# Kernel tuning notes

Measured on AMD Instinct MI355X. Metric: run time of the kernel, lower is better.

The kernel has to match this reference:

```python
import jax, jax.numpy as jnp
import numpy as np

DIM = 1024
HEADS = 16
HEAD_DIM = DIM // HEADS
EPS = 1e-5


def layer_norm(x, w, b):
    # normalize over last dim (head_dim)
    mu = jnp.mean(x, axis=-1, keepdims=True)
    var = jnp.mean(jnp.square(x - mu), axis=-1, keepdims=True)
    return (x - mu) * jax.lax.rsqrt(var + EPS) * w + b


def setup_inputs() -> dict:
    key = jax.random.key(0)
    ks = jax.random.split(key, 8)
    B, N = 2, 2048
    x = jax.random.normal(ks[0], (B, N, DIM), dtype=jnp.float32)
    mask = jax.random.randint(ks[1], (B, 1, N, N), 0, 2) == 1  # True = masked out
    qkv_w = jax.random.normal(ks[2], (3 * DIM, DIM), dtype=jnp.float32) * (DIM ** -0.5)
    q_norm_w = jnp.ones((HEAD_DIM,), dtype=jnp.float32)
    q_norm_b = jnp.zeros((HEAD_DIM,), dtype=jnp.float32)
    k_norm_w = jnp.ones((HEAD_DIM,), dtype=jnp.float32)
    k_norm_b = jnp.zeros((HEAD_DIM,), dtype=jnp.float32)
    proj_w = jax.random.normal(ks[3], (DIM, DIM), dtype=jnp.float32) * (DIM ** -0.5)
    proj_b = jnp.zeros((DIM,), dtype=jnp.float32)
    return {"x": x, "mask": mask, "qkv_w": qkv_w,
            "q_norm_w": q_norm_w, "q_norm_b": q_norm_b,
            "k_norm_w": k_norm_w, "k_norm_b": k_norm_b,
            "proj_w": proj_w, "proj_b": proj_b}


def reference(x, mask, qkv_w, q_norm_w, q_norm_b, k_norm_w, k_norm_b, proj_w, proj_b):
    B, N, C = x.shape
    H, D = HEADS, HEAD_DIM
    scale = D ** -0.5
    # qkv projection (no bias), split into q,k,v of shape (B,H,N,D)
    qkv = (x @ qkv_w.T).reshape(B, N, 3, H, D).transpose(2, 0, 3, 1, 4)
    q, k, v = qkv[0], qkv[1], qkv[2]
    q = layer_norm(q, q_norm_w, q_norm_b)
    k = layer_norm(k, k_norm_w, k_norm_b)
    q = q * scale
    attn = jnp.einsum("bhnd,bhmd->bhnm", q, k)  # (B,H,N,N)
    attn = jnp.where(mask, -jnp.inf, attn)
    attn = jax.nn.softmax(attn, axis=-1)
    out = jnp.einsum("bhnm,bhmd->bhnd", attn, v)
    out = out.transpose(0, 2, 1, 3).reshape(B, N, C)
    return out @ proj_w.T + proj_b
```

## Files before the change

kernel.cpp:

```cpp
#include <hip/hip_runtime.h>
#include <hip/hip_bf16.h>
#include <math.h>

#define B_    2
#define N_    2048
#define DIM_  1024
#define H_    16
#define HD_   64
#define EPS_  1e-5f
#define SCALE_ 0.125f

typedef __attribute__((ext_vector_type(8))) __bf16 bf16x8;
typedef __attribute__((ext_vector_type(8))) unsigned short ushort8;
typedef __attribute__((ext_vector_type(4))) float f32x4;

__device__ __forceinline__ unsigned short f2bf(float x) {
    unsigned u = __builtin_bit_cast(unsigned, x);
    u += 0x7fff + ((u >> 16) & 1);
    return (unsigned short)(u >> 16);
}
__device__ __forceinline__ float bf2f(unsigned short x) {
    unsigned u = ((unsigned)x) << 16;
    return __builtin_bit_cast(float, u);
}

__device__ __forceinline__ void gl_lds16(const void* g, void* l) {
    __builtin_amdgcn_global_load_lds(
        (const __attribute__((address_space(1))) void*)g,
        (__attribute__((address_space(3))) void*)l, 16, 0, 0);
}

__global__ __launch_bounds__(256) void cast_all_bf16(
    const float* __restrict__ x, const float* __restrict__ qkvw,
    const float* __restrict__ pw, unsigned short* __restrict__ out) {
    int i = (blockIdx.x * 256 + threadIdx.x) * 8;
    const float* src;
    if (i < 4194304) src = x + i;
    else if (i < 7340032) src = qkvw + (i - 4194304);
    else src = pw + (i - 7340032);
    float4 v0 = *(const float4*)src;
    float4 v1 = *(const float4*)(src + 4);
    ushort8 r;
    r[0] = f2bf(v0.x); r[1] = f2bf(v0.y); r[2] = f2bf(v0.z); r[3] = f2bf(v0.w);
    r[4] = f2bf(v1.x); r[5] = f2bf(v1.y); r[6] = f2bf(v1.z); r[7] = f2bf(v1.w);
    *(ushort8*)(out + i) = r;
}

__global__ __launch_bounds__(256) void pack_mask(
    const int* __restrict__ mask, unsigned long long* __restrict__ bm) {
    int w = blockIdx.x * 4 + (threadIdx.x >> 6);
    int lane = threadIdx.x & 63;
    int mv = mask[(size_t)w * 64 + lane];
    unsigned long long bits = __ballot(mv != 0);
    if (lane == 0) bm[w] = bits;
}

template <int WITH_BIAS, int OUT_BF16>
__global__ __launch_bounds__(256) void gemm_bt_mfma(
    const unsigned short* __restrict__ A, const unsigned short* __restrict__ Bw,
    const float* __restrict__ bias, void* __restrict__ Cout, int M, int Ncols,
    int K) {
    __shared__ unsigned short As[128 * 32];
    __shared__ unsigned short Bs[128 * 32];
    const int tid = threadIdx.x;
    const int wave = tid >> 6, lane = tid & 63;
    const int quad = lane >> 4, lcol = lane & 15;
    const int wr = wave >> 1, wc = wave & 1;
    const int row0 = blockIdx.y * 128, col0 = blockIdx.x * 128;

    f32x4 acc[4][4];
#pragma unroll
    for (int i = 0; i < 4; ++i)
#pragma unroll
        for (int j = 0; j < 4; ++j) acc[i][j] = (f32x4){0.f, 0.f, 0.f, 0.f};

    for (int k0 = 0; k0 < K; k0 += 32) {
        __syncthreads();
#pragma unroll
        for (int c = 0; c < 2; ++c) {
            int base = wave * 2048 + c * 1024;
            int myofs = base + lane * 16;
            int r = myofs >> 6;
            int kb = myofs & 63;
            gl_lds16((const char*)A + ((size_t)(row0 + r) * K + k0) * 2 + kb,
                     (char*)As + base);
            gl_lds16((const char*)Bw + ((size_t)(col0 + r) * K + k0) * 2 + kb,
                     (char*)Bs + base);
        }
        __syncthreads();

        bf16x8 af[4], bfr[4];
#pragma unroll
        for (int i = 0; i < 4; ++i) {
            af[i] = *(const bf16x8*)&As[(wr * 64 + i * 16 + lcol) * 32 + quad * 8];
            bfr[i] = *(const bf16x8*)&Bs[(wc * 64 + i * 16 + lcol) * 32 + quad * 8];
        }
#pragma unroll
        for (int i = 0; i < 4; ++i)
#pragma unroll
            for (int j = 0; j < 4; ++j)
                acc[i][j] = __builtin_amdgcn_mfma_f32_16x16x32_bf16(
                    af[i], bfr[j], acc[i][j], 0, 0, 0);
    }

#pragma unroll
    for (int i = 0; i < 4; ++i) {
#pragma unroll
        for (int j = 0; j < 4; ++j) {
            int col = col0 + wc * 64 + j * 16 + lcol;
            float bv = WITH_BIAS ? bias[col] : 0.f;
#pragma unroll
            for (int reg = 0; reg < 4; ++reg) {
                int row = row0 + wr * 64 + i * 16 + quad * 4 + reg;
                float v = acc[i][j][reg] + bv;
                if (OUT_BF16)
                    ((unsigned short*)Cout)[(size_t)row * Ncols + col] = f2bf(v);
                else
                    ((float*)Cout)[(size_t)row * Ncols + col] = v;
            }
        }
    }
}

__global__ __launch_bounds__(256) void qkv_norm_split(
    const unsigned short* __restrict__ qkv, const float* __restrict__ qw,
    const float* __restrict__ qb, const float* __restrict__ kw,
    const float* __restrict__ kb, unsigned short* __restrict__ qo,
    unsigned short* __restrict__ ko) {
    int wid = blockIdx.x * 4 + (threadIdx.x >> 6);
    int lane = threadIdx.x & 63;
    int h = wid & 15;
    int t = (wid >> 4) & 1;
    int bn = wid >> 5;
    int n = bn & (N_ - 1);
    int b = bn >> 11;
    float val = bf2f(qkv[((size_t)bn * 3 + t) * DIM_ + h * 64 + lane]);
    size_t oidx = ((size_t)(b * H_ + h) * N_ + n) * 64 + lane;
    float s = val;
#pragma unroll
    for (int off = 32; off > 0; off >>= 1) s += __shfl_xor(s, off);
    float mu = s * (1.f / 64.f);
    float d = val - mu;
    float s2 = d * d;
#pragma unroll
    for (int off = 32; off > 0; off >>= 1) s2 += __shfl_xor(s2, off);
    float r = rsqrtf(s2 * (1.f / 64.f) + EPS_);
    if (t == 0) {
        qo[oidx] = f2bf((d * r * qw[lane] + qb[lane]) * SCALE_);
    } else {
        ko[oidx] = f2bf(d * r * kw[lane] + kb[lane]);
    }
}

__global__ __launch_bounds__(256) void transpose_v(
    const unsigned short* __restrict__ qkv, unsigned short* __restrict__ vt) {
    __shared__ unsigned short Ts[64 * 65];
    const int tid = threadIdx.x;
    const int bh = blockIdx.y, n0 = blockIdx.x * 64;
    const int b = bh >> 4, h = bh & 15;
    {
        int r = tid >> 2, s = tid & 3;
        const unsigned short* src =
            qkv + ((size_t)(b * N_ + n0 + r) * 3 + 2) * DIM_ + h * 64 + s * 16;
#pragma unroll
        for (int i = 0; i < 16; ++i) Ts[r * 65 + s * 16 + i] = src[i];
    }
    __syncthreads();
    {
        int d = tid >> 2, ks = tid & 3;
        __align__(16) unsigned short tmp[16];
#pragma unroll
        for (int i = 0; i < 16; ++i) tmp[i] = Ts[(ks * 16 + i) * 65 + d];
        unsigned short* dst = vt + (size_t)(bh * 64 + d) * N_ + n0 + ks * 16;
        *(int4*)dst = *(const int4*)&tmp[0];
        *(int4*)(dst + 8) = *(const int4*)&tmp[8];
    }
}

__global__ __launch_bounds__(256) void flash_attn_mfma3(
    const unsigned short* __restrict__ q, const unsigned short* __restrict__ k,
    const unsigned short* __restrict__ vt,
    const unsigned long long* __restrict__ bm, unsigned short* __restrict__ ao) {
    __shared__ unsigned short Qs[128 * 64];
    __shared__ unsigned short Ks[64 * 64];
    __shared__ unsigned short Vts[64 * 64];
    __shared__ unsigned short Ps[4][32 * 72];

    const int tid = threadIdx.x;
    const int wave = tid >> 6, lane = tid & 63;
    const int quad = lane >> 4, lcol = lane & 15;
    const int bh = blockIdx.y, b = bh >> 4, h = bh & 15;
    const int q0 = blockIdx.x * 128;

    {
        const char* qg = (const char*)(q + (size_t)(bh * N_ + q0) * 64);
#pragma unroll
        for (int c = 0; c < 4; ++c) {
            int base = wave * 4096 + c * 1024;
            gl_lds16(qg + base + lane * 16, (char*)Qs + base);
        }
    }
    __syncthreads();

    bf16x8 bq[2][2];
#pragma unroll
    for (int ct = 0; ct < 2; ++ct)
#pragma unroll
        for (int d0 = 0; d0 < 2; ++d0)
            bq[ct][d0] = *(const bf16x8*)&Qs[(wave * 32 + ct * 16 + lcol) * 64 +
                                             d0 * 32 + quad * 8];

    f32x4 oacc[2][4];
    float m_c[2], l_c[2];
#pragma unroll
    for (int ct = 0; ct < 2; ++ct) {
#pragma unroll
        for (int dt = 0; dt < 4; ++dt) oacc[ct][dt] = (f32x4){0.f, 0.f, 0.f, 0.f};
        m_c[ct] = -3.0e38f;
        l_c[ct] = 0.f;
    }

    const unsigned long long* bmq[2];
#pragma unroll
    for (int ct = 0; ct < 2; ++ct)
        bmq[ct] = bm + ((size_t)b * N_ + q0 + wave * 32 + ct * 16 + lcol) * 32;

    const char* kgbase = (const char*)k + (size_t)bh * N_ * 128;
    const char* vtbase = (const char*)vt + (size_t)bh * 64 * N_ * 2;

    for (int k0 = 0; k0 < N_; k0 += 64) {
        __syncthreads();
#pragma unroll
        for (int ci = 0; ci < 2; ++ci) {
            int c = wave * 2 + ci;
            int swz = (c & 3) * 2;
            int key = lane ^ swz;
            gl_lds16(kgbase + (size_t)(k0 + key) * 128 + c * 16,
                     (char*)Ks + c * 1024);
            int d = lane ^ swz;
            gl_lds16(vtbase + ((size_t)d * N_ + k0 + c * 8) * 2,
                     (char*)Vts + c * 1024);
        }
        unsigned long long mw[2];
        const int widx = k0 >> 6;
        mw[0] = bmq[0][widx];
        mw[1] = bmq[1][widx];
        __syncthreads();

        f32x4 sacc[2][4];
#pragma unroll
        for (int ct = 0; ct < 2; ++ct)
#pragma unroll
            for (int kt = 0; kt < 4; ++kt) sacc[ct][kt] = (f32x4){0.f, 0.f, 0.f, 0.f};
#pragma unroll
        for (int kt = 0; kt < 4; ++kt) {
#pragma unroll
            for (int d0 = 0; d0 < 2; ++d0) {
                int p = d0 * 4 + quad;
                bf16x8 ak = *(const bf16x8*)((const char*)Ks + p * 1024 +
                                             (((kt * 16 + lcol) ^ (quad * 2)) << 4));
#pragma unroll
                for (int ct = 0; ct < 2; ++ct)
                    sacc[ct][kt] = __builtin_amdgcn_mfma_f32_16x16x32_bf16(
                        ak, bq[ct][d0], sacc[ct][kt], 0, 0, 0);
            }
        }

#pragma unroll
        for (int ct = 0; ct < 2; ++ct) {
            unsigned long long mq = mw[ct] >> (quad * 4);
            float mloc = -3.0e38f;
#pragma unroll
            for (int kt = 0; kt < 4; ++kt) {
                unsigned nib = (unsigned)(mq >> (kt * 16)) & 0xFu;
#pragma unroll
                for (int reg = 0; reg < 4; ++reg) {
                    float s = ((nib >> reg) & 1u) ? -1e30f : sacc[ct][kt][reg];
                    sacc[ct][kt][reg] = s;
                    mloc = fmaxf(mloc, s);
                }
            }
            mloc = fmaxf(mloc, __shfl_xor(mloc, 16));
            mloc = fmaxf(mloc, __shfl_xor(mloc, 32));
            float mold = m_c[ct];
            float mnew = fmaxf(mold, mloc);
            float alpha = __expf(mold - mnew);
            m_c[ct] = mnew;
            float rs = 0.f;
#pragma unroll
            for (int kt = 0; kt < 4; ++kt) {
                unsigned short us[4];
#pragma unroll
                for (int reg = 0; reg < 4; ++reg) {
                    float p = __expf(sacc[ct][kt][reg] - mnew);
                    rs += p;
                    us[reg] = f2bf(p);
                }
                uint2 pk;
                pk.x = us[0] | ((unsigned)us[1] << 16);
                pk.y = us[2] | ((unsigned)us[3] << 16);
                *(uint2*)&Ps[wave][(ct * 16 + lcol) * 72 + kt * 16 + quad * 4] = pk;
            }
            rs += __shfl_xor(rs, 16);
            rs += __shfl_xor(rs, 32);
            l_c[ct] = l_c[ct] * alpha + rs;
#pragma unroll
            for (int dt = 0; dt < 4; ++dt)
#pragma unroll
                for (int reg = 0; reg < 4; ++reg) oacc[ct][dt][reg] *= alpha;
        }

#pragma unroll
        for (int k2 = 0; k2 < 2; ++k2) {
            bf16x8 pf[2];
#pragma unroll
            for (int ct = 0; ct < 2; ++ct)
                pf[ct] = *(const bf16x8*)&Ps[wave][(ct * 16 + lcol) * 72 +
                                                   k2 * 32 + quad * 8];
#pragma unroll
            for (int dt = 0; dt < 4; ++dt) {
                int p = k2 * 4 + quad;
                bf16x8 vf = *(const bf16x8*)((const char*)Vts + p * 1024 +
                                             (((dt * 16 + lcol) ^ (quad * 2)) << 4));
#pragma unroll
                for (int ct = 0; ct < 2; ++ct)
                    oacc[ct][dt] = __builtin_amdgcn_mfma_f32_16x16x32_bf16(
                        vf, pf[ct], oacc[ct][dt], 0, 0, 0);
            }
        }
    }

#pragma unroll
    for (int ct = 0; ct < 2; ++ct) {
        float inv = 1.f / l_c[ct];
        int row = q0 + wave * 32 + ct * 16 + lcol;
        unsigned short* dst =
            ao + ((size_t)(b * N_ + row)) * DIM_ + h * 64 + quad * 4;
#pragma unroll
        for (int dt = 0; dt < 4; ++dt) {
            unsigned short us[4];
#pragma unroll
            for (int reg = 0; reg < 4; ++reg)
                us[reg] = f2bf(oacc[ct][dt][reg] * inv);
            uint2 pk;
            pk.x = us[0] | ((unsigned)us[1] << 16);
            pk.y = us[2] | ((unsigned)us[3] << 16);
            *(uint2*)(dst + dt * 16) = pk;
        }
    }
}

extern "C" void kernel_launch(void* const* d_in, const int* in_sizes, int n_in,
                              void* d_out, int out_size, void* d_ws,
                              size_t ws_size, hipStream_t stream) {
    const float* x     = (const float*)d_in[0];
    const int*   mask  = (const int*)d_in[1];
    const float* qkv_w = (const float*)d_in[2];
    const float* qnw   = (const float*)d_in[3];
    const float* qnb   = (const float*)d_in[4];
    const float* knw   = (const float*)d_in[5];
    const float* knb   = (const float*)d_in[6];
    const float* pw    = (const float*)d_in[7];
    const float* pb    = (const float*)d_in[8];
    float* out = (float*)d_out;

    char* ws = (char*)d_ws;
    unsigned short* qkv_bf = (unsigned short*)(ws + 0);
    unsigned short* qbuf   = (unsigned short*)(ws + 25165824);
    unsigned short* kbuf   = (unsigned short*)(ws + 33554432);
    unsigned short* vt     = (unsigned short*)(ws + 41943040);
    unsigned short* x_bf   = (unsigned short*)(ws + 50331648);
    unsigned short* qw_bf  = (unsigned short*)(ws + 58720256);
    unsigned short* pw_bf  = (unsigned short*)(ws + 65011712);
    unsigned short* ao_bnc = x_bf;
    unsigned long long* bmask = (unsigned long long*)(ws + 0);

    cast_all_bf16<<<8388608 / 2048, 256, 0, stream>>>(x, qkv_w, pw, x_bf);

    gemm_bt_mfma<0, 1><<<dim3(3072 / 128, 4096 / 128), 256, 0, stream>>>(
        x_bf, qw_bf, nullptr, qkv_bf, B_ * N_, 3 * DIM_, DIM_);

    qkv_norm_split<<<dim3((B_ * N_ * 2 * H_) / 4), 256, 0, stream>>>(
        qkv_bf, qnw, qnb, knw, knb, qbuf, kbuf);

    transpose_v<<<dim3(N_ / 64, B_ * H_), 256, 0, stream>>>(qkv_bf, vt);

    pack_mask<<<(B_ * N_ * (N_ / 64)) / 4, 256, 0, stream>>>(mask, bmask);

    flash_attn_mfma3<<<dim3(N_ / 128, B_ * H_), 256, 0, stream>>>(
        qbuf, kbuf, vt, bmask, ao_bnc);

    gemm_bt_mfma<1, 0><<<dim3(DIM_ / 128, 4096 / 128), 256, 0, stream>>>(
        ao_bnc, pw_bf, pb, out, B_ * N_, DIM_, DIM_);
}
```

Before: 304.7 us.

## Fuse QK layernorm into QKV GEMM epilogue and halve attention query tile

The QKV GEMM epilogue now computes the per-head layernorm for Q and K directly from accumulators and writes head-major Q/K buffers plus a separate V buffer. This removes the separate norm kernel and the round trip through the bf16 qkv buffer. The attention kernel drops from 128 to 64 query rows per block, which doubles the grid and cuts registers, at the cost of reloading K/V tiles twice as often. Softmax now uses exp2 with log2e folded into the Q scale, and bf16 packing uses a perm-based round (round-half-up rather than round-to-even).

```diff
diff --git a/kernel.cpp b/kernel.cpp
--- a/kernel.cpp
+++ b/kernel.cpp
@@ -9,6 +9,7 @@
 #define HD_   64
 #define EPS_  1e-5f
 #define SCALE_ 0.125f
+#define LOG2E_ 1.4426950408889634f
 
 typedef __attribute__((ext_vector_type(8))) __bf16 bf16x8;
 typedef __attribute__((ext_vector_type(8))) unsigned short ushort8;
@@ -19,9 +20,10 @@
     u += 0x7fff + ((u >> 16) & 1);
     return (unsigned short)(u >> 16);
 }
-__device__ __forceinline__ float bf2f(unsigned short x) {
-    unsigned u = ((unsigned)x) << 16;
-    return __builtin_bit_cast(float, u);
+__device__ __forceinline__ unsigned pk2bf(float a, float b) {
+    unsigned ua = __builtin_bit_cast(unsigned, a) + 0x8000u;
+    unsigned ub = __builtin_bit_cast(unsigned, b) + 0x8000u;
+    return __builtin_amdgcn_perm(ub, ua, 0x07060302);
 }
 
 __device__ __forceinline__ void gl_lds16(const void* g, void* l) {
@@ -55,6 +57,120 @@
     if (lane == 0) bm[w] = bits;
 }
 
+__global__ __launch_bounds__(256) void gemm_qkv_ln(
+    const unsigned short* __restrict__ A, const unsigned short* __restrict__ Bw,
+    const float* __restrict__ qnw, const float* __restrict__ qnb,
+    const float* __restrict__ knw, const float* __restrict__ knb,
+    unsigned short* __restrict__ qbuf, unsigned short* __restrict__ kbuf,
+    unsigned short* __restrict__ vbuf) {
+    const int K = DIM_;
+    __shared__ unsigned short As[128 * 32];
+    __shared__ unsigned short Bs[128 * 32];
+    const int tid = threadIdx.x;
+    const int wave = tid >> 6, lane = tid & 63;
+    const int quad = lane >> 4, lcol = lane & 15;
+    const int wr = wave >> 1, wc = wave & 1;
+    const int row0 = blockIdx.y * 128, col0 = blockIdx.x * 128;
+
+    f32x4 acc[4][4];
+#pragma unroll
+    for (int i = 0; i < 4; ++i)
+#pragma unroll
+        for (int j = 0; j < 4; ++j) acc[i][j] = (f32x4){0.f, 0.f, 0.f, 0.f};
+
+    for (int k0 = 0; k0 < K; k0 += 32) {
+        __syncthreads();
+#pragma unroll
+        for (int c = 0; c < 2; ++c) {
+            int base = wave * 2048 + c * 1024;
+            int myofs = base + lane * 16;
+            int r = myofs >> 6;
+            int kb = myofs & 63;
+            gl_lds16((const char*)A + ((size_t)(row0 + r) * K + k0) * 2 + kb,
+                     (char*)As + base);
+            gl_lds16((const char*)Bw + ((size_t)(col0 + r) * K + k0) * 2 + kb,
+                     (char*)Bs + base);
+        }
+        __syncthreads();
+
+        bf16x8 af[4], bfr[4];
+#pragma unroll
+        for (int i = 0; i < 4; ++i) {
+            af[i] = *(const bf16x8*)&As[(wr * 64 + i * 16 + lcol) * 32 + quad * 8];
+            bfr[i] = *(const bf16x8*)&Bs[(wc * 64 + i * 16 + lcol) * 32 + quad * 8];
+        }
+#pragma unroll
+        for (int i = 0; i < 4; ++i)
+#pragma unroll
+            for (int j = 0; j < 4; ++j)
+                acc[i][j] = __builtin_amdgcn_mfma_f32_16x16x32_bf16(
+                    af[i], bfr[j], acc[i][j], 0, 0, 0);
+    }
+
+    const int colbase = col0 + wc * 64;
+    const int t = colbase >> 10;
+    const int h = (colbase & 1023) >> 6;
+
+    if (t < 2) {
+        const float* wv = (t == 0) ? qnw : knw;
+        const float* bv = (t == 0) ? qnb : knb;
+        float wreg[4], breg[4];
+#pragma unroll
+        for (int j = 0; j < 4; ++j) {
+            wreg[j] = wv[j * 16 + lcol];
+            breg[j] = bv[j * 16 + lcol];
+        }
+        const float sc = (t == 0) ? (SCALE_ * LOG2E_) : 1.f;
+        unsigned short* obase = (t == 0) ? qbuf : kbuf;
+#pragma unroll
+        for (int i = 0; i < 4; ++i) {
+#pragma unroll
+            for (int reg = 0; reg < 4; ++reg) {
+                int row = row0 + wr * 64 + i * 16 + quad * 4 + reg;
+                int bb = row >> 11, n = row & (N_ - 1);
+                float v[4];
+#pragma unroll
+                for (int j = 0; j < 4; ++j) v[j] = acc[i][j][reg];
+                float s = v[0] + v[1] + v[2] + v[3];
+                s += __shfl_xor(s, 1);
+                s += __shfl_xor(s, 2);
+                s += __shfl_xor(s, 4);
+                s += __shfl_xor(s, 8);
+                float mu = s * (1.f / 64.f);
+                float d[4], s2 = 0.f;
+#pragma unroll
+                for (int j = 0; j < 4; ++j) {
+                    d[j] = v[j] - mu;
+                    s2 += d[j] * d[j];
+                }
+                s2 += __shfl_xor(s2, 1);
+                s2 += __shfl_xor(s2, 2);
+                s2 += __shfl_xor(s2, 4);
+                s2 += __shfl_xor(s2, 8);
+                float r = rsqrtf(s2 * (1.f / 64.f) + EPS_);
+                unsigned short* dst =
+                    obase + ((size_t)(bb * H_ + h) * N_ + n) * 64 + lcol;
+#pragma unroll
+                for (int j = 0; j < 4; ++j)
+                    dst[j * 16] = f2bf((d[j] * r * wreg[j] + breg[j]) * sc);
+            }
+        }
+    } else {
+        const int dcol = colbase & 1023;
+#pragma unroll
+        for (int i = 0; i < 4; ++i) {
+#pragma unroll
+            for (int reg = 0; reg < 4; ++reg) {
+                int row = row0 + wr * 64 + i * 16 + quad * 4 + reg;
+                unsigned short* dst = vbuf + (size_t)row * DIM_ + dcol + lcol;
+#pragma unroll
+                for (int j = 0; j < 4; ++j)
+                    dst[j * 16] = f2bf(acc[i][j][reg]);
+            }
+        }
+    }
+}
+
 template <int WITH_BIAS, int OUT_BF16>
 __global__ __launch_bounds__(256) void gemm_bt_mfma(
     const unsigned short* __restrict__ A, const unsigned short* __restrict__ Bw,
@@ -122,38 +238,8 @@
     }
 }
 
-__global__ __launch_bounds__(256) void qkv_norm_split(
-    const unsigned short* __restrict__ qkv, const float* __restrict__ qw,
-    const float* __restrict__ qb, const float* __restrict__ kw,
-    const float* __restrict__ kb, unsigned short* __restrict__ qo,
-    unsigned short* __restrict__ ko) {
-    int wid = blockIdx.x * 4 + (threadIdx.x >> 6);
-    int lane = threadIdx.x & 63;
-    int h = wid & 15;
-    int t = (wid >> 4) & 1;
-    int bn = wid >> 5;
-    int n = bn & (N_ - 1);
-    int b = bn >> 11;
-    float val = bf2f(qkv[((size_t)bn * 3 + t) * DIM_ + h * 64 + lane]);
-    size_t oidx = ((size_t)(b * H_ + h) * N_ + n) * 64 + lane;
-    float s = val;
-#pragma unroll
-    for (int off = 32; off > 0; off >>= 1) s += __shfl_xor(s, off);
-    float mu = s * (1.f / 64.f);
-    float d = val - mu;
-    float s2 = d * d;
-#pragma unroll
-    for (int off = 32; off > 0; off >>= 1) s2 += __shfl_xor(s2, off);
-    float r = rsqrtf(s2 * (1.f / 64.f) + EPS_);
-    if (t == 0) {
-        qo[oidx] = f2bf((d * r * qw[lane] + qb[lane]) * SCALE_);
-    } else {
-        ko[oidx] = f2bf(d * r * kw[lane] + kb[lane]);
-    }
-}
-
 __global__ __launch_bounds__(256) void transpose_v(
-    const unsigned short* __restrict__ qkv, unsigned short* __restrict__ vt) {
+    const unsigned short* __restrict__ vbuf, unsigned short* __restrict__ vt) {
     __shared__ unsigned short Ts[64 * 65];
     const int tid = threadIdx.x;
     const int bh = blockIdx.y, n0 = blockIdx.x * 64;
@@ -161,7 +247,7 @@
     {
         int r = tid >> 2, s = tid & 3;
         const unsigned short* src =
-            qkv + ((size_t)(b * N_ + n0 + r) * 3 + 2) * DIM_ + h * 64 + s * 16;
+            vbuf + (size_t)(b * N_ + n0 + r) * DIM_ + h * 64 + s * 16;
 #pragma unroll
         for (int i = 0; i < 16; ++i) Ts[r * 65 + s * 16 + i] = src[i];
     }
@@ -177,54 +263,43 @@
     }
 }
 
-__global__ __launch_bounds__(256) void flash_attn_mfma3(
+__global__ __launch_bounds__(256) void flash_attn_mfma4(
     const unsigned short* __restrict__ q, const unsigned short* __restrict__ k,
     const unsigned short* __restrict__ vt,
     const unsigned long long* __restrict__ bm, unsigned short* __restrict__ ao) {
-    __shared__ unsigned short Qs[128 * 64];
+    __shared__ unsigned short Qs[64 * 64];
     __shared__ unsigned short Ks[64 * 64];
     __shared__ unsigned short Vts[64 * 64];
-    __shared__ unsigned short Ps[4][32 * 72];
+    __shared__ unsigned short Ps[4][16 * 72];
 
     const int tid = threadIdx.x;
     const int wave = tid >> 6, lane = tid & 63;
     const int quad = lane >> 4, lcol = lane & 15;
     const int bh = blockIdx.y, b = bh >> 4, h = bh & 15;
-    const int q0 = blockIdx.x * 128;
+    const int q0 = blockIdx.x * 64;
 
     {
         const char* qg = (const char*)(q + (size_t)(bh * N_ + q0) * 64);
 #pragma unroll
-        for (int c = 0; c < 4; ++c) {
-            int base = wave * 4096 + c * 1024;
+        for (int c = 0; c < 2; ++c) {
+            int base = wave * 2048 + c * 1024;
             gl_lds16(qg + base + lane * 16, (char*)Qs + base);
         }
     }
     __syncthreads();
 
-    bf16x8 bq[2][2];
-#pragma unroll
-    for (int ct = 0; ct < 2; ++ct)
-#pragma unroll
-        for (int d0 = 0; d0 < 2; ++d0)
-            bq[ct][d0] = *(const bf16x8*)&Qs[(wave * 32 + ct * 16 + lcol) * 64 +
-                                             d0 * 32 + quad * 8];
-
-    f32x4 oacc[2][4];
-    float m_c[2], l_c[2];
-#pragma unroll
-    for (int ct = 0; ct < 2; ++ct) {
-#pragma unroll
-        for (int dt = 0; dt < 4; ++dt) oacc[ct][dt] = (f32x4){0.f, 0.f, 0.f, 0.f};
-        m_c[ct] = -3.0e38f;
-        l_c[ct] = 0.f;
-    }
-
-    const unsigned long long* bmq[2];
-#pragma unroll
-    for (int ct = 0; ct < 2; ++ct)
-        bmq[ct] = bm + ((size_t)b * N_ + q0 + wave * 32 + ct * 16 + lcol) * 32;
-
+    bf16x8 bq[2];
+#pragma unroll
+    for (int d0 = 0; d0 < 2; ++d0)
+        bq[d0] = *(const bf16x8*)&Qs[(wave * 16 + lcol) * 64 + d0 * 32 + quad * 8];
+
+    f32x4 oacc[4];
+#pragma unroll
+    for (int dt = 0; dt < 4; ++dt) oacc[dt] = (f32x4){0.f, 0.f, 0.f, 0.f};
+    float m_c = -3.0e38f, l_c = 0.f;
+
+    const unsigned long long* bmq =
+        bm + ((size_t)b * N_ + q0 + wave * 16 + lcol) * 32;
     const char* kgbase = (const char*)k + (size_t)bh * N_ * 128;
     const char* vtbase = (const char*)vt + (size_t)bh * 64 * N_ * 2;
 
@@ -241,17 +316,12 @@
             gl_lds16(vtbase + ((size_t)d * N_ + k0 + c * 8) * 2,
                      (char*)Vts + c * 1024);
         }
-        unsigned long long mw[2];
-        const int widx = k0 >> 6;
-        mw[0] = bmq[0][widx];
-        mw[1] = bmq[1][widx];
-        __syncthreads();
-
-        f32x4 sacc[2][4];
-#pragma unroll
-        for (int ct = 0; ct < 2; ++ct)
-#pragma unroll
-            for (int kt = 0; kt < 4; ++kt) sacc[ct][kt] = (f32x4){0.f, 0.f, 0.f, 0.f};
+        unsigned long long mw = bmq[k0 >> 6];
+        __syncthreads();
+
+        f32x4 sacc[4];
+#pragma unroll
+        for (int kt = 0; kt < 4; ++kt) sacc[kt] = (f32x4){0.f, 0.f, 0.f, 0.f};
 #pragma unroll
         for (int kt = 0; kt < 4; ++kt) {
 #pragma unroll
@@ -259,94 +329,73 @@
                 int p = d0 * 4 + quad;
                 bf16x8 ak = *(const bf16x8*)((const char*)Ks + p * 1024 +
                                              (((kt * 16 + lcol) ^ (quad * 2)) << 4));
-#pragma unroll
-                for (int ct = 0; ct < 2; ++ct)
-                    sacc[ct][kt] = __builtin_amdgcn_mfma_f32_16x16x32_bf16(
-                        ak, bq[ct][d0], sacc[ct][kt], 0, 0, 0);
-            }
-        }
-
-#pragma unroll
-        for (int ct = 0; ct < 2; ++ct) {
-            unsigned long long mq = mw[ct] >> (quad * 4);
-            float mloc = -3.0e38f;
-#pragma unroll
-            for (int kt = 0; kt < 4; ++kt) {
-                unsigned nib = (unsigned)(mq >> (kt * 16)) & 0xFu;
-#pragma unroll
-                for (int reg = 0; reg < 4; ++reg) {
-                    float s = ((nib >> reg) & 1u) ? -1e30f : sacc[ct][kt][reg];
-                    sacc[ct][kt][reg] = s;
-                    mloc = fmaxf(mloc, s);
-                }
-            }
-            mloc = fmaxf(mloc, __shfl_xor(mloc, 16));
-            mloc = fmaxf(mloc, __shfl_xor(mloc, 32));
-            float mold = m_c[ct];
-            float mnew = fmaxf(mold, mloc);
-            float alpha = __expf(mold - mnew);
-            m_c[ct] = mnew;
-            float rs = 0.f;
-#pragma unroll
-            for (int kt = 0; kt < 4; ++kt) {
-                unsigned short us[4];
-#pragma unroll
-                for (int reg = 0; reg < 4; ++reg) {
-                    float p = __expf(sacc[ct][kt][reg] - mnew);
-                    rs += p;
-                    us[reg] = f2bf(p);
-                }
-                uint2 pk;
-                pk.x = us[0] | ((unsigned)us[1] << 16);
-                pk.y = us[2] | ((unsigned)us[3] << 16);
-                *(uint2*)&Ps[wave][(ct * 16 + lcol) * 72 + kt * 16 + quad * 4] = pk;
-            }
-            rs += __shfl_xor(rs, 16);
-            rs += __shfl_xor(rs, 32);
-            l_c[ct] = l_c[ct] * alpha + rs;
-#pragma unroll
-            for (int dt = 0; dt < 4; ++dt)
-#pragma unroll
-                for (int reg = 0; reg < 4; ++reg) oacc[ct][dt][reg] *= alpha;
-        }
+                sacc[kt] = __builtin_amdgcn_mfma_f32_16x16x32_bf16(
+                    ak, bq[d0], sacc[kt], 0, 0, 0);
+            }
+        }
+
+        unsigned long long mq = mw >> (quad * 4);
+        float mloc = -3.0e38f;
+#pragma unroll
+        for (int kt = 0; kt < 4; ++kt) {
+            unsigned nib = (unsigned)(mq >> (kt * 16)) & 0xFu;
+#pragma unroll
+            for (int reg = 0; reg < 4; ++reg) {
+                float s = ((nib >> reg) & 1u) ? -1e30f : sacc[kt][reg];
+                sacc[kt][reg] = s;
+                mloc = fmaxf(mloc, s);
+            }
+        }
+        mloc = fmaxf(mloc, __shfl_xor(mloc, 16));
+        mloc = fmaxf(mloc, __shfl_xor(mloc, 32));
+        float mnew = fmaxf(m_c, mloc);
+        float alpha = exp2f(m_c - mnew);
+        m_c = mnew;
+        float rs = 0.f;
+#pragma unroll
+        for (int kt = 0; kt < 4; ++kt) {
+            float p0 = exp2f(sacc[kt][0] - mnew);
+            float p1 = exp2f(sacc[kt][1] - mnew);
+            float p2 = exp2f(sacc[kt][2] - mnew);
+            float p3 = exp2f(sacc[kt][3] - mnew);
+            rs += (p0 + p1) + (p2 + p3);
+            uint2 pk;
+            pk.x = pk2bf(p0, p1);
+            pk.y = pk2bf(p2, p3);
+            *(uint2*)&Ps[wave][lcol * 72 + kt * 16 + quad * 4] = pk;
+        }
+        rs += __shfl_xor(rs, 16);
+        rs += __shfl_xor(rs, 32);
+        l_c = l_c * alpha + rs;
+#pragma unroll
+        for (int dt = 0; dt < 4; ++dt)
+#pragma unroll
+            for (int reg = 0; reg < 4; ++reg) oacc[dt][reg] *= alpha;
 
 #pragma unroll
         for (int k2 = 0; k2 < 2; ++k2) {
-            bf16x8 pf[2];
-#pragma unroll
-            for (int ct = 0; ct < 2; ++ct)
-                pf[ct] = *(const bf16x8*)&Ps[wave][(ct * 16 + lcol) * 72 +
-                                                   k2 * 32 + quad * 8];
+            bf16x8 pf =
+                *(const bf16x8*)&Ps[wave][lcol * 72 + k2 * 32 + quad * 8];
 #pragma unroll
             for (int dt = 0; dt < 4; ++dt) {
                 int p = k2 * 4 + quad;
                 bf16x8 vf = *(const bf16x8*)((const char*)Vts + p * 1024 +
                                              (((dt * 16 + lcol) ^ (quad * 2)) << 4));
-#pragma unroll
-                for (int ct = 0; ct < 2; ++ct)
-                    oacc[ct][dt] = __builtin_amdgcn_mfma_f32_16x16x32_bf16(
-                        vf, pf[ct], oacc[ct][dt], 0, 0, 0);
-            }
-        }
-    }
-
-#pragma unroll
-    for (int ct = 0; ct < 2; ++ct) {
-        float inv = 1.f / l_c[ct];
-        int row = q0 + wave * 32 + ct * 16 + lcol;
-        unsigned short* dst =
-            ao + ((size_t)(b * N_ + row)) * DIM_ + h * 64 + quad * 4;
-#pragma unroll
-        for (int dt = 0; dt < 4; ++dt) {
-            unsigned short us[4];
-#pragma unroll
-            for (int reg = 0; reg < 4; ++reg)
-                us[reg] = f2bf(oacc[ct][dt][reg] * inv);
-            uint2 pk;
-            pk.x = us[0] | ((unsigned)us[1] << 16);
-            pk.y = us[2] | ((unsigned)us[3] << 16);
-            *(uint2*)(dst + dt * 16) = pk;
-        }
+                oacc[dt] = __builtin_amdgcn_mfma_f32_16x16x32_bf16(
+                    vf, pf, oacc[dt], 0, 0, 0);
+            }
+        }
+    }
+
+    float inv = 1.f / l_c;
+    int row = q0 + wave * 16 + lcol;
+    unsigned short* dst = ao + ((size_t)(b * N_ + row)) * DIM_ + h * 64 + quad * 4;
+#pragma unroll
+    for (int dt = 0; dt < 4; ++dt) {
+        uint2 pk;
+        pk.x = pk2bf(oacc[dt][0] * inv, oacc[dt][1] * inv);
+        pk.y = pk2bf(oacc[dt][2] * inv, oacc[dt][3] * inv);
+        *(uint2*)(dst + dt * 16) = pk;
     }
 }
 
@@ -365,29 +414,26 @@
     float* out = (float*)d_out;
 
     char* ws = (char*)d_ws;
-    unsigned short* qkv_bf = (unsigned short*)(ws + 0);
-    unsigned short* qbuf   = (unsigned short*)(ws + 25165824);
-    unsigned short* kbuf   = (unsigned short*)(ws + 33554432);
-    unsigned short* vt     = (unsigned short*)(ws + 41943040);
-    unsigned short* x_bf   = (unsigned short*)(ws + 50331648);
-    unsigned short* qw_bf  = (unsigned short*)(ws + 58720256);
-    unsigned short* pw_bf  = (unsigned short*)(ws + 65011712);
-    unsigned short* ao_bnc = x_bf;
-    unsigned long long* bmask = (unsigned long long*)(ws + 0);
+    unsigned short* x_bf  = (unsigned short*)(ws + 0);
+    unsigned short* qw_bf = (unsigned short*)(ws + 8388608);
+    unsigned short* pw_bf = (unsigned short*)(ws + 14680064);
+    unsigned short* qbuf  = (unsigned short*)(ws + 16777216);
+    unsigned short* kbuf  = (unsigned short*)(ws + 25165824);
+    unsigned short* vbuf  = (unsigned short*)(ws + 33554432);
+    unsigned short* vt    = (unsigned short*)(ws + 41943040);
+    unsigned long long* bmask = (unsigned long long*)(ws + 50331648);
+    unsigned short* ao_bnc = vbuf;
 
     cast_all_bf16<<<8388608 / 2048, 256, 0, stream>>>(x, qkv_w, pw, x_bf);
 
-    gemm_bt_mfma<0, 1><<<dim3(3072 / 128, 4096 / 128), 256, 0, stream>>>(
-        x_bf, qw_bf, nullptr, qkv_bf, B_ * N_, 3 * DIM_, DIM_);
-
-    qkv_norm_split<<<dim3((B_ * N_ * 2 * H_) / 4), 256, 0, stream>>>(
-        qkv_bf, qnw, qnb, knw, knb, qbuf, kbuf);
-
-    transpose_v<<<dim3(N_ / 64, B_ * H_), 256, 0, stream>>>(qkv_bf, vt);
+    gemm_qkv_ln<<<dim3(3072 / 128, 4096 / 128), 256, 0, stream>>>(
+        x_bf, qw_bf, qnw, qnb, knw, knb, qbuf, kbuf, vbuf);
+
+    transpose_v<<<dim3(N_ / 64, B_ * H_), 256, 0, stream>>>(vbuf, vt);
 
     pack_mask<<<(B_ * N_ * (N_ / 64)) / 4, 256, 0, stream>>>(mask, bmask);
 
-    flash_attn_mfma3<<<dim3(N_ / 128, B_ * H_), 256, 0, stream>>>(
+    flash_attn_mfma4<<<dim3(N_ / 64, B_ * H_), 256, 0, stream>>>(
         qbuf, kbuf, vt, bmask, ao_bnc);
 
     gemm_bt_mfma<1, 0><<<dim3(DIM_ / 128, 4096 / 128), 256, 0, stream>>>(
```

After: 298.2 us. 1.02x faster.
